# Optimization experiments

Hardware: AMD Instinct MI355X
Metric: run time of the kernel (lower is better)

## Reference

```python
import jax, jax.numpy as jnp
import numpy as np

N = 100000
E = 1000000
IN_DIM = 128
HID = 128
OUT_DIM = 64
HEADS = 4
NEG_SLOPE = 0.2


def _glorot(key, shape, fan_in, fan_out):
    lim = np.sqrt(6.0 / (fan_in + fan_out))
    return jax.random.uniform(key, shape, jnp.float32, -lim, lim)


def setup_inputs() -> dict:
    key = jax.random.key(0)
    ks = jax.random.split(key, 16)
    x = jax.random.normal(ks[0], (N, IN_DIM), jnp.float32)
    edge_index = jax.random.randint(ks[1], (2, E), 0, N, jnp.int32)
    # layer 0: in 128 -> 4 heads x 32 (concat)
    W0 = _glorot(ks[2], (IN_DIM, HEADS * (HID // HEADS)), IN_DIM, HID)
    as0 = _glorot(ks[3], (HEADS, HID // HEADS), HID // HEADS, 1)
    ad0 = _glorot(ks[4], (HEADS, HID // HEADS), HID // HEADS, 1)
    b0 = jnp.zeros((HID,), jnp.float32)
    # layer 1: 128 -> 4 heads x 32 (concat)
    W1 = _glorot(ks[5], (HID, HEADS * (HID // HEADS)), HID, HID)
    as1 = _glorot(ks[6], (HEADS, HID // HEADS), HID // HEADS, 1)
    ad1 = _glorot(ks[7], (HEADS, HID // HEADS), HID // HEADS, 1)
    b1 = jnp.zeros((HID,), jnp.float32)
    # layer 2: 128 -> 1 head x 64 (no concat)
    W2 = _glorot(ks[8], (HID, OUT_DIM), HID, OUT_DIM)
    as2 = _glorot(ks[9], (1, OUT_DIM), OUT_DIM, 1)
    ad2 = _glorot(ks[10], (1, OUT_DIM), OUT_DIM, 1)
    b2 = jnp.zeros((OUT_DIM,), jnp.float32)
    return {"x": x, "edge_index": edge_index,
            "W0": W0, "as0": as0, "ad0": ad0, "b0": b0,
            "W1": W1, "as1": as1, "ad1": ad1, "b1": b1,
            "W2": W2, "as2": as2, "ad2": ad2, "b2": b2}


def gat_conv(x, src, dst, W, a_src, a_dst, b, heads, out_ch, concat):
    n = x.shape[0]
    h = (x @ W).reshape(n, heads, out_ch)              # [N,H,C]
    al_s = jnp.einsum('nhc,hc->nh', h, a_src)           # [N,H]
    al_d = jnp.einsum('nhc,hc->nh', h, a_dst)           # [N,H]
    e = jax.nn.leaky_relu(al_s[src] + al_d[dst], NEG_SLOPE)   # [Etot,H]
    e_max = jax.ops.segment_max(e, dst, num_segments=n)        # [N,H]
    w = jnp.exp(e - e_max[dst])                                 # [Etot,H]
    denom = jax.ops.segment_sum(w, dst, num_segments=n)        # [N,H]
    msg = w[:, :, None] * h[src]                                # [Etot,H,C]
    out = jax.ops.segment_sum(msg, dst, num_segments=n)        # [N,H,C]
    out = out / (denom[:, :, None] + 1e-16)
    out = out.reshape(n, heads * out_ch) if concat else out.mean(axis=1)
    return out + b


def reference(x, edge_index, W0, as0, ad0, b0, W1, as1, ad1, b1, W2, as2, ad2, b2):
    # add self loops (PyG GATConv default add_self_loops=True)
    loops = jnp.arange(N, dtype=edge_index.dtype)
    src = jnp.concatenate([edge_index[0], loops])
    dst = jnp.concatenate([edge_index[1], loops])
    h = gat_conv(x, src, dst, W0, as0, ad0, b0, HEADS, HID // HEADS, True)
    h = jax.nn.elu(h)  # dropout is identity at eval
    h = gat_conv(h, src, dst, W1, as1, ad1, b1, HEADS, HID // HEADS, True)
    h = jax.nn.elu(h)
    out = gat_conv(h, src, dst, W2, as2, ad2, b2, 1, OUT_DIM, False)
    return out
```

## Files before the change

kernel.cpp:

```cpp
#include <hip/hip_runtime.h>
#include <hip/hip_bf16.h>
#include <math.h>

#define N_NODES 100000
#define N_EDGES 1000000
#define ETOT    (N_EDGES + N_NODES)

#define NBUCK 391
#define BCAP  3584
#define EPB_A 4096

constexpr float NEG_SLOPE = 0.2f;

typedef short short8 __attribute__((ext_vector_type(8)));
typedef float f32x4  __attribute__((ext_vector_type(4)));
typedef unsigned short ushort_t;
typedef unsigned int uint_t;
typedef long long ll_t;

__device__ __forceinline__ ushort_t f2bf(float f) {
    uint_t u = __float_as_uint(f);
    u += 0x7fff + ((u >> 16) & 1);
    return (ushort_t)(u >> 16);
}
__device__ __forceinline__ float bf2f(ushort_t h) {
    return __uint_as_float((uint_t)h << 16);
}
__device__ __forceinline__ float bf2f_lo(uint_t v) { return __uint_as_float(v << 16); }
__device__ __forceinline__ float bf2f_hi(uint_t v) { return __uint_as_float(v & 0xffff0000u); }

__global__ void binit_kernel(int* __restrict__ bcur) {
    int b = blockIdx.x * blockDim.x + threadIdx.x;
    if (b < NBUCK) bcur[b] = b * BCAP;
}

__global__ __launch_bounds__(256) void bucketA_kernel(const int* __restrict__ ei,
                                                      int* __restrict__ bcur,
                                                      ll_t* __restrict__ pairs) {
    __shared__ ll_t spair[EPB_A];
    __shared__ int  sgpos[EPB_A];
    __shared__ int  hist[NBUCK];
    __shared__ int  hscan[NBUCK];
    __shared__ int  base[NBUCK];
    __shared__ int  cur2[NBUCK];
    __shared__ int  sc[512];

    const int t = threadIdx.x;
    const int e0 = blockIdx.x * EPB_A;
    const int nvalid = min(EPB_A, ETOT - e0);

    for (int b = t; b < NBUCK; b += 256) { hist[b] = 0; cur2[b] = 0; }
    __syncthreads();

    for (int r = 0; r < EPB_A / 256; r++) {
        int i = e0 + r * 256 + t;
        if (i < ETOT) {
            int dst = (i < N_EDGES) ? ei[N_EDGES + i] : (i - N_EDGES);
            atomicAdd(&hist[dst >> 8], 1);
        }
    }
    __syncthreads();

    sc[t]       = (t < NBUCK) ? hist[t] : 0;
    sc[t + 256] = (t + 256 < NBUCK) ? hist[t + 256] : 0;
    __syncthreads();
    for (int off = 1; off < 512; off <<= 1) {
        int v0 = (t >= off) ? sc[t - off] : 0;
        int v1 = sc[t + 256 - off];
        __syncthreads();
        sc[t] += v0;
        sc[t + 256] += v1;
        __syncthreads();
    }
    for (int b = t; b < NBUCK; b += 256) {
        hscan[b] = sc[b] - hist[b];
        if (hist[b] > 0) base[b] = atomicAdd(&bcur[b], hist[b]);
    }
    __syncthreads();

    for (int r = 0; r < EPB_A / 256; r++) {
        int i = e0 + r * 256 + t;
        if (i < ETOT) {
            int src, dst;
            if (i < N_EDGES) { src = ei[i]; dst = ei[N_EDGES + i]; }
            else             { src = dst = i - N_EDGES; }
            int b = dst >> 8;
            int lr = atomicAdd(&cur2[b], 1);
            int slot = hscan[b] + lr;
            spair[slot] = ((ll_t)dst << 32) | (uint_t)src;
            sgpos[slot] = base[b] + lr;
        }
    }
    __syncthreads();

    for (int s = t; s < nvalid; s += 256)
        pairs[sgpos[s]] = spair[s];
}

__global__ __launch_bounds__(256) void bucketB1_kernel(const ll_t* __restrict__ pairs,
                                                       const int* __restrict__ bcur,
                                                       int* __restrict__ counts) {
    __shared__ int h[256];
    const int b = blockIdx.x, t = threadIdx.x;
    h[t] = 0;
    __syncthreads();
    const int cnt = bcur[b] - b * BCAP;
    for (int i = t; i < cnt; i += 256) {
        int dst = (int)(pairs[(size_t)b * BCAP + i] >> 32);
        atomicAdd(&h[dst & 255], 1);
    }
    __syncthreads();
    int node = b * 256 + t;
    if (node < N_NODES) counts[node] = h[t];
}

__global__ __launch_bounds__(256) void bucketB2_kernel(const ll_t* __restrict__ pairs,
                                                       const int* __restrict__ bcur,
                                                       const int* __restrict__ offs,
                                                       int* __restrict__ csr) {
    __shared__ int cur[256];
    const int b = blockIdx.x, t = threadIdx.x;
    int node = b * 256 + t;
    cur[t] = (node < N_NODES) ? offs[node] : 0;
    __syncthreads();
    const int cnt = bcur[b] - b * BCAP;
    for (int i = t; i < cnt; i += 256) {
        ll_t p = pairs[(size_t)b * BCAP + i];
        int src = (int)(p & 0xffffffff);
        int dst = (int)(p >> 32);
        int pos = atomicAdd(&cur[dst & 255], 1);
        csr[pos] = src;
    }
}

__global__ __launch_bounds__(256) void block_sum_kernel(const int* __restrict__ counts,
                                                        int* __restrict__ blockSums, int n) {
    int b = blockIdx.x, t = threadIdx.x;
    int base = b * 1024 + t * 4;
    int s = 0;
    if (base + 3 < n) {
        int4 v = *reinterpret_cast<const int4*>(counts + base);
        s = v.x + v.y + v.z + v.w;
    } else {
        for (int i = 0; i < 4; i++) if (base + i < n) s += counts[base + i];
    }
    #pragma unroll
    for (int off = 32; off > 0; off >>= 1) s += __shfl_down(s, off);
    __shared__ int wsum[4];
    int lane = t & 63, wv = t >> 6;
    if (lane == 0) wsum[wv] = s;
    __syncthreads();
    if (t == 0) blockSums[b] = wsum[0] + wsum[1] + wsum[2] + wsum[3];
}

__global__ __launch_bounds__(256) void scan_sums_kernel(const int* __restrict__ blockSums,
                                                        int* __restrict__ blockBase, int nb) {
    __shared__ int sh[256];
    int t = threadIdx.x;
    int v = (t < nb) ? blockSums[t] : 0;
    sh[t] = v;
    __syncthreads();
    for (int off = 1; off < 256; off <<= 1) {
        int u = (t >= off) ? sh[t - off] : 0;
        __syncthreads();
        sh[t] += u;
        __syncthreads();
    }
    if (t < nb) blockBase[t] = sh[t] - v;
}

__global__ __launch_bounds__(256) void scan_final_kernel(const int* __restrict__ counts,
                                                         const int* __restrict__ blockBase,
                                                         int* __restrict__ offsets, int n) {
    int b = blockIdx.x, t = threadIdx.x;
    int base = b * 1024 + t * 4;
    int c[4] = {0, 0, 0, 0};
    if (base + 3 < n) {
        int4 v = *reinterpret_cast<const int4*>(counts + base);
        c[0] = v.x; c[1] = v.y; c[2] = v.z; c[3] = v.w;
    } else {
        for (int i = 0; i < 4; i++) if (base + i < n) c[i] = counts[base + i];
    }
    int tsum = c[0] + c[1] + c[2] + c[3];
    int x = tsum;
    int lane = t & 63, wv = t >> 6;
    #pragma unroll
    for (int off = 1; off < 64; off <<= 1) {
        int u = __shfl_up(x, off);
        if (lane >= off) x += u;
    }
    __shared__ int wsum[4];
    if (lane == 63) wsum[wv] = x;
    __syncthreads();
    int wbase = 0;
    for (int w = 0; w < wv; w++) wbase += wsum[w];
    int run = blockBase[b] + wbase + (x - tsum);
    for (int i = 0; i < 4; i++) {
        if (base + i < n) { offsets[base + i] = run; run += c[i]; }
    }
    if (b == 0 && t == 0) offsets[n] = ETOT;
}

template <int OUT, int H, bool IN_BF16>
__global__ __launch_bounds__(256) void gemm_mfma(const void* __restrict__ Xv,
                                                 const float* __restrict__ W,
                                                 const float* __restrict__ a_s,
                                                 const float* __restrict__ a_d,
                                                 ushort_t* __restrict__ Hout,
                                                 float* __restrict__ alS,
                                                 float* __restrict__ alD, int nrows) {
    constexpr int NB  = OUT / 16;
    constexpr int CPH = OUT / H;
    constexpr int TPH = NB / H;
    __shared__ ushort_t Wt[OUT * 128];
    const int t = threadIdx.x;

    {
        constexpr int GROUPS = 256 / OUT;
        constexpr int KPG    = 128 / GROUPS;
        int col = t & (OUT - 1);
        int kb0 = (t / OUT) * KPG;
        for (int c = 0; c < KPG / 8; c++) {
            int kb = kb0 + c * 8;
            short8 v;
            #pragma unroll
            for (int j = 0; j < 8; j++) v[j] = (short)f2bf(W[(kb + j) * OUT + col]);
            int off = col * 256 + (((kb >> 3) << 4) ^ ((col & 15) << 4));
            *reinterpret_cast<short8*>(reinterpret_cast<char*>(Wt) + off) = v;
        }
    }
    __syncthreads();

    const int wv = t >> 6, lane = t & 63;
    const int rowBase = (blockIdx.x * 4 + wv) * 32;
    if (rowBase >= nrows) return;
    const int r0 = lane & 15, g = lane >> 4;

    f32x4 acc[2][NB];
    #pragma unroll
    for (int rt = 0; rt < 2; rt++)
        #pragma unroll
        for (int nb = 0; nb < NB; nb++) acc[rt][nb] = {0.f, 0.f, 0.f, 0.f};

    #pragma unroll
    for (int step = 0; step < 4; step++) {
        short8 a0, a1;
        if (IN_BF16) {
            const ushort_t* X = (const ushort_t*)Xv;
            a0 = *reinterpret_cast<const short8*>(X + (size_t)(rowBase + r0) * 128 + step * 32 + g * 8);
            a1 = *reinterpret_cast<const short8*>(X + (size_t)(rowBase + 16 + r0) * 128 + step * 32 + g * 8);
        } else {
            const float* X = (const float*)Xv;
            const float* p0 = X + (size_t)(rowBase + r0) * 128 + step * 32 + g * 8;
            const float* p1 = X + (size_t)(rowBase + 16 + r0) * 128 + step * 32 + g * 8;
            #pragma unroll
            for (int j = 0; j < 8; j++) { a0[j] = (short)f2bf(p0[j]); a1[j] = (short)f2bf(p1[j]); }
        }
        const int chunkoff = (step << 6) + (g << 4);
        #pragma unroll
        for (int nb = 0; nb < NB; nb++) {
            int col = nb * 16 + r0;
            int off = col * 256 + (chunkoff ^ (r0 << 4));
            short8 b = *reinterpret_cast<const short8*>(reinterpret_cast<const char*>(Wt) + off);
            acc[0][nb] = __builtin_amdgcn_mfma_f32_16x16x32_bf16(a0, b, acc[0][nb], 0, 0, 0);
            acc[1][nb] = __builtin_amdgcn_mfma_f32_16x16x32_bf16(a1, b, acc[1][nb], 0, 0, 0);
        }
    }

    #pragma unroll
    for (int rt = 0; rt < 2; rt++) {
        #pragma unroll
        for (int nb = 0; nb < NB; nb++) {
            #pragma unroll
            for (int rr = 0; rr < 4; rr++) {
                int row = rowBase + rt * 16 + g * 4 + rr;
                Hout[(size_t)row * OUT + nb * 16 + r0] = f2bf(acc[rt][nb][rr]);
            }
        }
    }

    float asv[NB], adv[NB];
    #pragma unroll
    for (int nb = 0; nb < NB; nb++) {
        int col = nb * 16 + r0;
        int h = col / CPH, c = col % CPH;
        asv[nb] = a_s[h * CPH + c];
        adv[nb] = a_d[h * CPH + c];
    }
    #pragma unroll
    for (int rt = 0; rt < 2; rt++) {
        #pragma unroll
        for (int rr = 0; rr < 4; rr++) {
            int row = rowBase + rt * 16 + g * 4 + rr;
            #pragma unroll
            for (int h = 0; h < H; h++) {
                float vs = 0.f, vd = 0.f;
                #pragma unroll
                for (int tt = 0; tt < TPH; tt++) {
                    int nb = h * TPH + tt;
                    vs += acc[rt][nb][rr] * asv[nb];
                    vd += acc[rt][nb][rr] * adv[nb];
                }
                #pragma unroll
                for (int off = 8; off > 0; off >>= 1) {
                    vs += __shfl_xor(vs, off, 16);
                    vd += __shfl_xor(vd, off, 16);
                }
                if (r0 == 0) {
                    alS[row * H + h] = vs;
                    alD[row * H + h] = vd;
                }
            }
        }
    }
}

template <bool DO_ELU>
__global__ __launch_bounds__(256) void agg128_sp(const ushort_t* __restrict__ Hf,
                                                 const float* __restrict__ alS,
                                                 const float* __restrict__ alD,
                                                 const float* __restrict__ bias,
                                                 const int* __restrict__ offs,
                                                 const int* __restrict__ csr,
                                                 ushort_t* __restrict__ out, int n) {
    int wave = (blockIdx.x * blockDim.x + threadIdx.x) >> 6;
    int lane = threadIdx.x & 63;
    if (wave >= n) return;
    const int node = wave;
    const int s0 = offs[node], s1 = offs[node + 1];
    const int hh = lane >> 4;
    const float aldn = alD[node * 4 + hh];

    float acc0 = 0.f, acc1 = 0.f, dacc = 0.f;

    int i = s0;
    for (; i + 3 < s1; i += 4) {
        int sa = csr[i], sb = csr[i + 1], sc_ = csr[i + 2], sd = csr[i + 3];
        float ea = alS[sa * 4 + hh], eb = alS[sb * 4 + hh];
        float ec = alS[sc_ * 4 + hh], ed = alS[sd * 4 + hh];
        uint_t va = *reinterpret_cast<const uint_t*>(Hf + (size_t)sa * 128 + lane * 2);
        uint_t vb = *reinterpret_cast<const uint_t*>(Hf + (size_t)sb * 128 + lane * 2);
        uint_t vc = *reinterpret_cast<const uint_t*>(Hf + (size_t)sc_ * 128 + lane * 2);
        uint_t vd = *reinterpret_cast<const uint_t*>(Hf + (size_t)sd * 128 + lane * 2);
        ea += aldn; ea = (ea > 0.f) ? ea : NEG_SLOPE * ea; float wa = __expf(ea);
        eb += aldn; eb = (eb > 0.f) ? eb : NEG_SLOPE * eb; float wb = __expf(eb);
        ec += aldn; ec = (ec > 0.f) ? ec : NEG_SLOPE * ec; float wc = __expf(ec);
        ed += aldn; ed = (ed > 0.f) ? ed : NEG_SLOPE * ed; float wd = __expf(ed);
        acc0 += wa * bf2f_lo(va); acc1 += wa * bf2f_hi(va);
        acc0 += wb * bf2f_lo(vb); acc1 += wb * bf2f_hi(vb);
        acc0 += wc * bf2f_lo(vc); acc1 += wc * bf2f_hi(vc);
        acc0 += wd * bf2f_lo(vd); acc1 += wd * bf2f_hi(vd);
        dacc += (wa + wb) + (wc + wd);
    }
    for (; i < s1; i++) {
        int sa = csr[i];
        float ea = alS[sa * 4 + hh];
        uint_t va = *reinterpret_cast<const uint_t*>(Hf + (size_t)sa * 128 + lane * 2);
        ea += aldn; ea = (ea > 0.f) ? ea : NEG_SLOPE * ea; float wa = __expf(ea);
        acc0 += wa * bf2f_lo(va); acc1 += wa * bf2f_hi(va);
        dacc += wa;
    }

    float rd = 1.0f / dacc;
    float o0 = acc0 * rd + bias[2 * lane];
    float o1 = acc1 * rd + bias[2 * lane + 1];
    if (DO_ELU) {
        o0 = (o0 > 0.0f) ? o0 : expm1f(o0);
        o1 = (o1 > 0.0f) ? o1 : expm1f(o1);
    }
    uint_t packed = (uint_t)f2bf(o0) | ((uint_t)f2bf(o1) << 16);
    *reinterpret_cast<uint_t*>(out + (size_t)node * 128 + lane * 2) = packed;
}

__global__ __launch_bounds__(256) void agg64_sp(const ushort_t* __restrict__ Hf,
                                                const float* __restrict__ alS,
                                                const float* __restrict__ alD,
                                                const float* __restrict__ bias,
                                                const int* __restrict__ offs,
                                                const int* __restrict__ csr,
                                                float* __restrict__ out, int n) {
    int wave = (blockIdx.x * blockDim.x + threadIdx.x) >> 6;
    int lane = threadIdx.x & 63;
    if (wave >= n) return;
    const int node = wave;
    const int s0 = offs[node], s1 = offs[node + 1];
    const float aldn = alD[node];

    const int eh = lane >> 5;
    const int c2 = lane & 31;
    float acc0 = 0.f, acc1 = 0.f, dacc = 0.f;

    int i = s0;
    for (; i + 3 < s1; i += 4) {
        int sa = csr[i + eh];
        int sb = csr[i + 2 + eh];
        float ea = alS[sa], eb = alS[sb];
        uint_t va = *reinterpret_cast<const uint_t*>(Hf + (size_t)sa * 64 + c2 * 2);
        uint_t vb = *reinterpret_cast<const uint_t*>(Hf + (size_t)sb * 64 + c2 * 2);
        ea += aldn; ea = (ea > 0.f) ? ea : NEG_SLOPE * ea; float wa = __expf(ea);
        eb += aldn; eb = (eb > 0.f) ? eb : NEG_SLOPE * eb; float wb = __expf(eb);
        acc0 += wa * bf2f_lo(va); acc1 += wa * bf2f_hi(va);
        acc0 += wb * bf2f_lo(vb); acc1 += wb * bf2f_hi(vb);
        dacc += wa + wb;
    }
    for (; i < s1; i += 2) {
        int idx = i + eh;
        if (idx < s1) {
            int sa = csr[idx];
            float ea = alS[sa];
            uint_t va = *reinterpret_cast<const uint_t*>(Hf + (size_t)sa * 64 + c2 * 2);
            ea += aldn; ea = (ea > 0.f) ? ea : NEG_SLOPE * ea; float wa = __expf(ea);
            acc0 += wa * bf2f_lo(va); acc1 += wa * bf2f_hi(va);
            dacc += wa;
        }
    }

    acc0 += __shfl_xor(acc0, 32);
    acc1 += __shfl_xor(acc1, 32);
    dacc += __shfl_xor(dacc, 32);
    if (lane < 32) {
        float rd = 1.0f / dacc;
        float2 o;
        o.x = acc0 * rd + bias[2 * c2];
        o.y = acc1 * rd + bias[2 * c2 + 1];
        *reinterpret_cast<float2*>(out + (size_t)node * 64 + c2 * 2) = o;
    }
}

extern "C" void kernel_launch(void* const* d_in, const int* in_sizes, int n_in,
                              void* d_out, int out_size, void* d_ws, size_t ws_size,
                              hipStream_t stream) {
    const float* x   = (const float*)d_in[0];
    const int*   ei  = (const int*)d_in[1];
    const float* W0  = (const float*)d_in[2];
    const float* as0 = (const float*)d_in[3];
    const float* ad0 = (const float*)d_in[4];
    const float* b0  = (const float*)d_in[5];
    const float* W1  = (const float*)d_in[6];
    const float* as1 = (const float*)d_in[7];
    const float* ad1 = (const float*)d_in[8];
    const float* b1  = (const float*)d_in[9];
    const float* W2  = (const float*)d_in[10];
    const float* as2 = (const float*)d_in[11];
    const float* ad2 = (const float*)d_in[12];
    const float* b2  = (const float*)d_in[13];

    char* ws = (char*)d_ws;
    size_t off = 0;
    auto alloc = [&](size_t bytes) -> void* {
        void* p = ws + off;
        off += (bytes + 255) & ~size_t(255);
        return p;
    };
    ushort_t* B0   = (ushort_t*)alloc((size_t)N_NODES * 128 * sizeof(ushort_t));
    ushort_t* B1   = (ushort_t*)alloc((size_t)N_NODES * 128 * sizeof(ushort_t));
    float* alS     = (float*)alloc((size_t)N_NODES * 4 * sizeof(float));
    float* alD     = (float*)alloc((size_t)N_NODES * 4 * sizeof(float));
    int*   counts  = (int*)alloc((size_t)N_NODES * sizeof(int));
    int*   offs    = (int*)alloc((size_t)(N_NODES + 1) * sizeof(int));
    int*   csr     = (int*)alloc((size_t)ETOT * sizeof(int));
    int*   bsums   = (int*)alloc(256 * sizeof(int));
    int*   bbase   = (int*)alloc(256 * sizeof(int));
    int*   bcur    = (int*)alloc((size_t)NBUCK * sizeof(int));
    ll_t*  pairs   = (ll_t*)alloc((size_t)NBUCK * BCAP * sizeof(ll_t));

    const int NB = (N_NODES + 1023) / 1024;

    binit_kernel<<<(NBUCK + 255) / 256, 256, 0, stream>>>(bcur);
    bucketA_kernel<<<(ETOT + EPB_A - 1) / EPB_A, 256, 0, stream>>>(ei, bcur, pairs);
    bucketB1_kernel<<<NBUCK, 256, 0, stream>>>(pairs, bcur, counts);
    block_sum_kernel<<<NB, 256, 0, stream>>>(counts, bsums, N_NODES);
    scan_sums_kernel<<<1, 256, 0, stream>>>(bsums, bbase, NB);
    scan_final_kernel<<<NB, 256, 0, stream>>>(counts, bbase, offs, N_NODES);
    bucketB2_kernel<<<NBUCK, 256, 0, stream>>>(pairs, bcur, offs, csr);

    const int GEMM_GRID = (N_NODES / 32 + 3) / 4;
    const int NODE_WAVE_GRID = (N_NODES + 3) / 4;

    gemm_mfma<128, 4, false><<<GEMM_GRID, 256, 0, stream>>>(x, W0, as0, ad0, B0, alS, alD, N_NODES);
    agg128_sp<true><<<NODE_WAVE_GRID, 256, 0, stream>>>(B0, alS, alD, b0, offs, csr, B1, N_NODES);

    gemm_mfma<128, 4, true><<<GEMM_GRID, 256, 0, stream>>>(B1, W1, as1, ad1, B0, alS, alD, N_NODES);
    agg128_sp<true><<<NODE_WAVE_GRID, 256, 0, stream>>>(B0, alS, alD, b1, offs, csr, B1, N_NODES);

    gemm_mfma<64, 1, true><<<GEMM_GRID, 256, 0, stream>>>(B1, W2, as2, ad2, B0, alS, alD, N_NODES);
    agg64_sp<<<NODE_WAVE_GRID, 256, 0, stream>>>(B0, alS, alD, b2, offs, csr,
                                                 (float*)d_out, N_NODES);
}
```

Measured before the change: 398.7 us.

## Pack bucket pairs into 32 bits and fold CSR scan into bucket kernels

Edge pairs are packed as src<<8 | local dst into 32-bit words instead of 64-bit, which halves the bucket scratch traffic. The per-node count/scan chain of three kernels is replaced by a per-bucket local scan in bucketB1, a tiny scan over bucket totals, and offset emission inside bucketB2, so fewer kernels are launched. Attention logits are prescaled by log2(e) in the GEMM so the aggregation kernels can use exp2 with fmax-based leaky ReLU. The rest are 32-bit indexing and vectorised bias loads; src<<8 relies on node ids fitting in 24 bits.

```diff
diff --git a/kernel.cpp b/kernel.cpp
--- a/kernel.cpp
+++ b/kernel.cpp
@@ -11,23 +11,28 @@
 #define EPB_A 4096
 
 constexpr float NEG_SLOPE = 0.2f;
+constexpr float LOG2E = 1.4426950408889634f;
 
 typedef short short8 __attribute__((ext_vector_type(8)));
 typedef float f32x4  __attribute__((ext_vector_type(4)));
 typedef unsigned short ushort_t;
 typedef unsigned int uint_t;
-typedef long long ll_t;
 
 __device__ __forceinline__ ushort_t f2bf(float f) {
     uint_t u = __float_as_uint(f);
     u += 0x7fff + ((u >> 16) & 1);
     return (ushort_t)(u >> 16);
 }
-__device__ __forceinline__ float bf2f(ushort_t h) {
-    return __uint_as_float((uint_t)h << 16);
-}
 __device__ __forceinline__ float bf2f_lo(uint_t v) { return __uint_as_float(v << 16); }
 __device__ __forceinline__ float bf2f_hi(uint_t v) { return __uint_as_float(v & 0xffff0000u); }
+
+__device__ __forceinline__ float exp2_fast(float x) {
+#if __has_builtin(__builtin_amdgcn_exp2f)
+    return __builtin_amdgcn_exp2f(x);
+#else
+    return exp2f(x);
+#endif
+}
 
 __global__ void binit_kernel(int* __restrict__ bcur) {
     int b = blockIdx.x * blockDim.x + threadIdx.x;
@@ -36,8 +41,8 @@
 
 __global__ __launch_bounds__(256) void bucketA_kernel(const int* __restrict__ ei,
                                                       int* __restrict__ bcur,
-                                                      ll_t* __restrict__ pairs) {
-    __shared__ ll_t spair[EPB_A];
+                                                      uint_t* __restrict__ pairs) {
+    __shared__ uint_t spair[EPB_A];
     __shared__ int  sgpos[EPB_A];
     __shared__ int  hist[NBUCK];
     __shared__ int  hscan[NBUCK];
@@ -87,7 +92,7 @@
             int b = dst >> 8;
             int lr = atomicAdd(&cur2[b], 1);
             int slot = hscan[b] + lr;
-            spair[slot] = ((ll_t)dst << 32) | (uint_t)src;
+            spair[slot] = ((uint_t)src << 8) | (uint_t)(dst & 255);
             sgpos[slot] = base[b] + lr;
         }
     }
@@ -97,108 +102,76 @@
         pairs[sgpos[s]] = spair[s];
 }
 
-__global__ __launch_bounds__(256) void bucketB1_kernel(const ll_t* __restrict__ pairs,
+__global__ __launch_bounds__(256) void bucketB1_kernel(const uint_t* __restrict__ pairs,
                                                        const int* __restrict__ bcur,
-                                                       int* __restrict__ counts) {
+                                                       int* __restrict__ localoff,
+                                                       int* __restrict__ btot) {
     __shared__ int h[256];
+    __shared__ int ws[4];
     const int b = blockIdx.x, t = threadIdx.x;
     h[t] = 0;
     __syncthreads();
     const int cnt = bcur[b] - b * BCAP;
-    for (int i = t; i < cnt; i += 256) {
-        int dst = (int)(pairs[(size_t)b * BCAP + i] >> 32);
-        atomicAdd(&h[dst & 255], 1);
-    }
-    __syncthreads();
-    int node = b * 256 + t;
-    if (node < N_NODES) counts[node] = h[t];
-}
-
-__global__ __launch_bounds__(256) void bucketB2_kernel(const ll_t* __restrict__ pairs,
+    for (int i = t; i < cnt; i += 256)
+        atomicAdd(&h[pairs[b * BCAP + i] & 255u], 1);
+    __syncthreads();
+    int c = h[t];
+    int lane = t & 63, wv = t >> 6;
+    int x = c;
+    #pragma unroll
+    for (int off = 1; off < 64; off <<= 1) {
+        int u = __shfl_up(x, off);
+        if (lane >= off) x += u;
+    }
+    if (lane == 63) ws[wv] = x;
+    __syncthreads();
+    int wb = 0;
+    for (int w = 0; w < wv; w++) wb += ws[w];
+    localoff[b * 256 + t] = wb + x - c;
+    if (t == 255) btot[b] = wb + x;
+}
+
+__global__ __launch_bounds__(256) void scanB_kernel(const int* __restrict__ btot,
+                                                    int* __restrict__ bbase,
+                                                    int* __restrict__ offs) {
+    __shared__ int sc[512];
+    int t = threadIdx.x;
+    int v0 = (t < NBUCK) ? btot[t] : 0;
+    int v1 = (t + 256 < NBUCK) ? btot[t + 256] : 0;
+    sc[t] = v0; sc[t + 256] = v1;
+    __syncthreads();
+    for (int off = 1; off < 512; off <<= 1) {
+        int u0 = (t >= off) ? sc[t - off] : 0;
+        int u1 = sc[t + 256 - off];
+        __syncthreads();
+        sc[t] += u0;
+        sc[t + 256] += u1;
+        __syncthreads();
+    }
+    if (t < NBUCK) bbase[t] = sc[t] - v0;
+    if (t + 256 < NBUCK) bbase[t + 256] = sc[t + 256] - v1;
+    if (t == 0) offs[N_NODES] = ETOT;
+}
+
+__global__ __launch_bounds__(256) void bucketB2_kernel(const uint_t* __restrict__ pairs,
                                                        const int* __restrict__ bcur,
-                                                       const int* __restrict__ offs,
+                                                       const int* __restrict__ localoff,
+                                                       const int* __restrict__ bbase,
+                                                       int* __restrict__ offs,
                                                        int* __restrict__ csr) {
     __shared__ int cur[256];
     const int b = blockIdx.x, t = threadIdx.x;
-    int node = b * 256 + t;
-    cur[t] = (node < N_NODES) ? offs[node] : 0;
+    const int node = b * 256 + t;
+    const int my = bbase[b] + localoff[b * 256 + t];
+    cur[t] = my;
+    if (node < N_NODES) offs[node] = my;
     __syncthreads();
     const int cnt = bcur[b] - b * BCAP;
     for (int i = t; i < cnt; i += 256) {
-        ll_t p = pairs[(size_t)b * BCAP + i];
-        int src = (int)(p & 0xffffffff);
-        int dst = (int)(p >> 32);
-        int pos = atomicAdd(&cur[dst & 255], 1);
-        csr[pos] = src;
-    }
-}
-
-__global__ __launch_bounds__(256) void block_sum_kernel(const int* __restrict__ counts,
-                                                        int* __restrict__ blockSums, int n) {
-    int b = blockIdx.x, t = threadIdx.x;
-    int base = b * 1024 + t * 4;
-    int s = 0;
-    if (base + 3 < n) {
-        int4 v = *reinterpret_cast<const int4*>(counts + base);
-        s = v.x + v.y + v.z + v.w;
-    } else {
-        for (int i = 0; i < 4; i++) if (base + i < n) s += counts[base + i];
-    }
-    #pragma unroll
-    for (int off = 32; off > 0; off >>= 1) s += __shfl_down(s, off);
-    __shared__ int wsum[4];
-    int lane = t & 63, wv = t >> 6;
-    if (lane == 0) wsum[wv] = s;
-    __syncthreads();
-    if (t == 0) blockSums[b] = wsum[0] + wsum[1] + wsum[2] + wsum[3];
-}
-
-__global__ __launch_bounds__(256) void scan_sums_kernel(const int* __restrict__ blockSums,
-                                                        int* __restrict__ blockBase, int nb) {
-    __shared__ int sh[256];
-    int t = threadIdx.x;
-    int v = (t < nb) ? blockSums[t] : 0;
-    sh[t] = v;
-    __syncthreads();
-    for (int off = 1; off < 256; off <<= 1) {
-        int u = (t >= off) ? sh[t - off] : 0;
-        __syncthreads();
-        sh[t] += u;
-        __syncthreads();
-    }
-    if (t < nb) blockBase[t] = sh[t] - v;
-}
-
-__global__ __launch_bounds__(256) void scan_final_kernel(const int* __restrict__ counts,
-                                                         const int* __restrict__ blockBase,
-                                                         int* __restrict__ offsets, int n) {
-    int b = blockIdx.x, t = threadIdx.x;
-    int base = b * 1024 + t * 4;
-    int c[4] = {0, 0, 0, 0};
-    if (base + 3 < n) {
-        int4 v = *reinterpret_cast<const int4*>(counts + base);
-        c[0] = v.x; c[1] = v.y; c[2] = v.z; c[3] = v.w;
-    } else {
-        for (int i = 0; i < 4; i++) if (base + i < n) c[i] = counts[base + i];
-    }
-    int tsum = c[0] + c[1] + c[2] + c[3];
-    int x = tsum;
-    int lane = t & 63, wv = t >> 6;
-    #pragma unroll
-    for (int off = 1; off < 64; off <<= 1) {
-        int u = __shfl_up(x, off);
-        if (lane >= off) x += u;
-    }
-    __shared__ int wsum[4];
-    if (lane == 63) wsum[wv] = x;
-    __syncthreads();
-    int wbase = 0;
-    for (int w = 0; w < wv; w++) wbase += wsum[w];
-    int run = blockBase[b] + wbase + (x - tsum);
-    for (int i = 0; i < 4; i++) {
-        if (base + i < n) { offsets[base + i] = run; run += c[i]; }
-    }
-    if (b == 0 && t == 0) offsets[n] = ETOT;
+        uint_t p = pairs[b * BCAP + i];
+        int pos = atomicAdd(&cur[p & 255u], 1);
+        csr[pos] = (int)(p >> 8);
+    }
 }
 
 template <int OUT, int H, bool IN_BF16>
@@ -307,8 +280,8 @@
                     vd += __shfl_xor(vd, off, 16);
                 }
                 if (r0 == 0) {
-                    alS[row * H + h] = vs;
-                    alD[row * H + h] = vd;
+                    alS[row * H + h] = vs * LOG2E;
+                    alD[row * H + h] = vd * LOG2E;
                 }
             }
         }
@@ -330,6 +303,7 @@
     const int s0 = offs[node], s1 = offs[node + 1];
     const int hh = lane >> 4;
     const float aldn = alD[node * 4 + hh];
+    const uint_t* __restrict__ Hf32 = (const uint_t*)Hf;
 
     float acc0 = 0.f, acc1 = 0.f, dacc = 0.f;
 
@@ -338,14 +312,14 @@
         int sa = csr[i], sb = csr[i + 1], sc_ = csr[i + 2], sd = csr[i + 3];
         float ea = alS[sa * 4 + hh], eb = alS[sb * 4 + hh];
         float ec = alS[sc_ * 4 + hh], ed = alS[sd * 4 + hh];
-        uint_t va = *reinterpret_cast<const uint_t*>(Hf + (size_t)sa * 128 + lane * 2);
-        uint_t vb = *reinterpret_cast<const uint_t*>(Hf + (size_t)sb * 128 + lane * 2);
-        uint_t vc = *reinterpret_cast<const uint_t*>(Hf + (size_t)sc_ * 128 + lane * 2);
-        uint_t vd = *reinterpret_cast<const uint_t*>(Hf + (size_t)sd * 128 + lane * 2);
-        ea += aldn; ea = (ea > 0.f) ? ea : NEG_SLOPE * ea; float wa = __expf(ea);
-        eb += aldn; eb = (eb > 0.f) ? eb : NEG_SLOPE * eb; float wb = __expf(eb);
-        ec += aldn; ec = (ec > 0.f) ? ec : NEG_SLOPE * ec; float wc = __expf(ec);
-        ed += aldn; ed = (ed > 0.f) ? ed : NEG_SLOPE * ed; float wd = __expf(ed);
+        uint_t va = Hf32[sa * 64 + lane];
+        uint_t vb = Hf32[sb * 64 + lane];
+        uint_t vc = Hf32[sc_ * 64 + lane];
+        uint_t vd = Hf32[sd * 64 + lane];
+        ea += aldn; float wa = exp2_fast(fmaxf(ea, NEG_SLOPE * ea));
+        eb += aldn; float wb = exp2_fast(fmaxf(eb, NEG_SLOPE * eb));
+        ec += aldn; float wc = exp2_fast(fmaxf(ec, NEG_SLOPE * ec));
+        ed += aldn; float wd = exp2_fast(fmaxf(ed, NEG_SLOPE * ed));
         acc0 += wa * bf2f_lo(va); acc1 += wa * bf2f_hi(va);
         acc0 += wb * bf2f_lo(vb); acc1 += wb * bf2f_hi(vb);
         acc0 += wc * bf2f_lo(vc); acc1 += wc * bf2f_hi(vc);
@@ -355,21 +329,22 @@
     for (; i < s1; i++) {
         int sa = csr[i];
         float ea = alS[sa * 4 + hh];
-        uint_t va = *reinterpret_cast<const uint_t*>(Hf + (size_t)sa * 128 + lane * 2);
-        ea += aldn; ea = (ea > 0.f) ? ea : NEG_SLOPE * ea; float wa = __expf(ea);
+        uint_t va = Hf32[sa * 64 + lane];
+        ea += aldn; float wa = exp2_fast(fmaxf(ea, NEG_SLOPE * ea));
         acc0 += wa * bf2f_lo(va); acc1 += wa * bf2f_hi(va);
         dacc += wa;
     }
 
     float rd = 1.0f / dacc;
-    float o0 = acc0 * rd + bias[2 * lane];
-    float o1 = acc1 * rd + bias[2 * lane + 1];
+    float2 bv = *reinterpret_cast<const float2*>(bias + 2 * lane);
+    float o0 = acc0 * rd + bv.x;
+    float o1 = acc1 * rd + bv.y;
     if (DO_ELU) {
         o0 = (o0 > 0.0f) ? o0 : expm1f(o0);
         o1 = (o1 > 0.0f) ? o1 : expm1f(o1);
     }
     uint_t packed = (uint_t)f2bf(o0) | ((uint_t)f2bf(o1) << 16);
-    *reinterpret_cast<uint_t*>(out + (size_t)node * 128 + lane * 2) = packed;
+    *reinterpret_cast<uint_t*>(out + node * 128 + lane * 2) = packed;
 }
 
 __global__ __launch_bounds__(256) void agg64_sp(const ushort_t* __restrict__ Hf,
@@ -385,6 +360,7 @@
     const int node = wave;
     const int s0 = offs[node], s1 = offs[node + 1];
     const float aldn = alD[node];
+    const uint_t* __restrict__ Hf32 = (const uint_t*)Hf;
 
     const int eh = lane >> 5;
     const int c2 = lane & 31;
@@ -395,10 +371,10 @@
         int sa = csr[i + eh];
         int sb = csr[i + 2 + eh];
         float ea = alS[sa], eb = alS[sb];
-        uint_t va = *reinterpret_cast<const uint_t*>(Hf + (size_t)sa * 64 + c2 * 2);
-        uint_t vb = *reinterpret_cast<const uint_t*>(Hf + (size_t)sb * 64 + c2 * 2);
-        ea += aldn; ea = (ea > 0.f) ? ea : NEG_SLOPE * ea; float wa = __expf(ea);
-        eb += aldn; eb = (eb > 0.f) ? eb : NEG_SLOPE * eb; float wb = __expf(eb);
+        uint_t va = Hf32[sa * 32 + c2];
+        uint_t vb = Hf32[sb * 32 + c2];
+        ea += aldn; float wa = exp2_fast(fmaxf(ea, NEG_SLOPE * ea));
+        eb += aldn; float wb = exp2_fast(fmaxf(eb, NEG_SLOPE * eb));
         acc0 += wa * bf2f_lo(va); acc1 += wa * bf2f_hi(va);
         acc0 += wb * bf2f_lo(vb); acc1 += wb * bf2f_hi(vb);
         dacc += wa + wb;
@@ -408,8 +384,8 @@
         if (idx < s1) {
             int sa = csr[idx];
             float ea = alS[sa];
-            uint_t va = *reinterpret_cast<const uint_t*>(Hf + (size_t)sa * 64 + c2 * 2);
-            ea += aldn; ea = (ea > 0.f) ? ea : NEG_SLOPE * ea; float wa = __expf(ea);
+            uint_t va = Hf32[sa * 32 + c2];
+            ea += aldn; float wa = exp2_fast(fmaxf(ea, NEG_SLOPE * ea));
             acc0 += wa * bf2f_lo(va); acc1 += wa * bf2f_hi(va);
             dacc += wa;
         }
@@ -420,10 +396,11 @@
     dacc += __shfl_xor(dacc, 32);
     if (lane < 32) {
         float rd = 1.0f / dacc;
+        float2 bv = *reinterpret_cast<const float2*>(bias + 2 * c2);
         float2 o;
-        o.x = acc0 * rd + bias[2 * c2];
-        o.y = acc1 * rd + bias[2 * c2 + 1];
-        *reinterpret_cast<float2*>(out + (size_t)node * 64 + c2 * 2) = o;
+        o.x = acc0 * rd + bv.x;
+        o.y = acc1 * rd + bv.y;
+        *reinterpret_cast<float2*>(out + node * 64 + c2 * 2) = o;
     }
 }
 
@@ -456,23 +433,19 @@
     ushort_t* B1   = (ushort_t*)alloc((size_t)N_NODES * 128 * sizeof(ushort_t));
     float* alS     = (float*)alloc((size_t)N_NODES * 4 * sizeof(float));
     float* alD     = (float*)alloc((size_t)N_NODES * 4 * sizeof(float));
-    int*   counts  = (int*)alloc((size_t)N_NODES * sizeof(int));
+    int*   localoff= (int*)alloc((size_t)(NBUCK * 256) * sizeof(int));
     int*   offs    = (int*)alloc((size_t)(N_NODES + 1) * sizeof(int));
     int*   csr     = (int*)alloc((size_t)ETOT * sizeof(int));
-    int*   bsums   = (int*)alloc(256 * sizeof(int));
-    int*   bbase   = (int*)alloc(256 * sizeof(int));
+    int*   btot    = (int*)alloc(512 * sizeof(int));
+    int*   bbase   = (int*)alloc(512 * sizeof(int));
     int*   bcur    = (int*)alloc((size_t)NBUCK * sizeof(int));
-    ll_t*  pairs   = (ll_t*)alloc((size_t)NBUCK * BCAP * sizeof(ll_t));
-
-    const int NB = (N_NODES + 1023) / 1024;
+    uint_t* pairs  = (uint_t*)alloc((size_t)NBUCK * BCAP * sizeof(uint_t));
 
     binit_kernel<<<(NBUCK + 255) / 256, 256, 0, stream>>>(bcur);
     bucketA_kernel<<<(ETOT + EPB_A - 1) / EPB_A, 256, 0, stream>>>(ei, bcur, pairs);
-    bucketB1_kernel<<<NBUCK, 256, 0, stream>>>(pairs, bcur, counts);
-    block_sum_kernel<<<NB, 256, 0, stream>>>(counts, bsums, N_NODES);
-    scan_sums_kernel<<<1, 256, 0, stream>>>(bsums, bbase, NB);
-    scan_final_kernel<<<NB, 256, 0, stream>>>(counts, bbase, offs, N_NODES);
-    bucketB2_kernel<<<NBUCK, 256, 0, stream>>>(pairs, bcur, offs, csr);
+    bucketB1_kernel<<<NBUCK, 256, 0, stream>>>(pairs, bcur, localoff, btot);
+    scanB_kernel<<<1, 256, 0, stream>>>(btot, bbase, offs);
+    bucketB2_kernel<<<NBUCK, 256, 0, stream>>>(pairs, bcur, localoff, bbase, offs, csr);
 
     const int GEMM_GRID = (N_NODES / 32 + 3) / 4;
     const int NODE_WAVE_GRID = (N_NODES + 3) / 4;
```

Result: no change. 391.0 us (-1.9%).
